# Performance work log

Hardware: AMD Instinct MI355X
Metric: run time of the kernel (lower is better)

## Reference

```python
import jax, jax.numpy as jnp
import numpy as np

NEG_INF = -9e15  # matches the torch -9000000000000000.0 mask value
LRELU_SLOPE = 0.01  # torch nn.LeakyReLU default


def setup_inputs() -> dict:
    key = jax.random.key(0)
    k1, k2, k3, k4 = jax.random.split(key, 4)
    N, F_in, F_out = 8192, 256, 128
    x = jax.random.normal(k1, (N, F_in), dtype=jnp.float32)
    adj = jax.random.randint(k2, (N, N), 0, 2, dtype=jnp.int32)
    # xavier_uniform with gain=1.414
    limW = 1.414 * np.sqrt(6.0 / (F_in + F_out))
    W = jax.random.uniform(k3, (F_in, F_out), minval=-limW, maxval=limW, dtype=jnp.float32)
    lima = 1.414 * np.sqrt(6.0 / (2 * F_out + 1))
    a = jax.random.uniform(k4, (2 * F_out, 1), minval=-lima, maxval=lima, dtype=jnp.float32)
    return {"x": x, "adj": adj, "W": W, "a": a}


def reference(x, adj, W, a):
    # h: [N, F_out]
    h = x @ W
    F_out = h.shape[1]
    a1 = a[:F_out, 0]   # attention vector for source node i
    a2 = a[F_out:, 0]   # attention vector for target node j
    # e[i, j] = leaky_relu(h_i . a1 + h_j . a2) -- equivalent to the repeat/cat
    # construction without materializing the [N, N, 2F] tensor.
    e = (h @ a1)[:, None] + (h @ a2)[None, :]  # [N, N]
    e = jnp.where(e > 0, e, LRELU_SLOPE * e)
    scores = jnp.where(adj > 0, e, NEG_INF)
    attention = jax.nn.softmax(scores, axis=1)  # dropout omitted (eval mode)
    h_prime = attention @ h  # [N, F_out]
    return jax.nn.elu(h_prime)
```

## Files before the change

kernel.cpp:

```cpp
#include <hip/hip_runtime.h>
#include <hip/hip_bf16.h>
#include <stdint.h>


#define N_NODES 8192
#define F_INF   256
#define F_OUT   128
#define LRELU   0.01f

typedef __bf16 bf16x8 __attribute__((ext_vector_type(8)));
typedef float  f32x4  __attribute__((ext_vector_type(4)));
using bf16 = __hip_bfloat16;

__device__ __forceinline__ float b2f(bf16 v) { return __bfloat162float(v); }
__device__ __forceinline__ bf16  f2b(float v) { return __float2bfloat16(v); }

__device__ __forceinline__ void gll16(const void* g, void* l) {
    __builtin_amdgcn_global_load_lds(
        (const __attribute__((address_space(1))) uint32_t*)g,
        (__attribute__((address_space(3))) uint32_t*)l, 16, 0, 0);
}

__global__ __launch_bounds__(256) void k_xw(const float* __restrict__ x,
                                            const float* __restrict__ W,
                                            const float* __restrict__ a,
                                            bf16* __restrict__ hT,
                                            float* __restrict__ s1,
                                            float* __restrict__ s2,
                                            float* __restrict__ mgp) {
    __shared__ __align__(16) bf16 WTh[F_OUT][F_INF + 8];
    __shared__ __align__(16) bf16 WTl[F_OUT][F_INF + 8];
    __shared__ __align__(16) bf16 XSh[32][72];
    __shared__ __align__(16) bf16 XSl[32][72];
    __shared__ float a1s[F_OUT], a2s[F_OUT], s1L[32], s2L[32];
    const int tid  = threadIdx.x;
    const int lane = tid & 63, wave = tid >> 6;
    const int i0   = blockIdx.x * 32;
    if (tid < F_OUT) { a1s[tid] = a[tid]; a2s[tid] = a[tid + F_OUT]; }
    if (tid < 32)    { s1L[tid] = 0.f; s2L[tid] = 0.f; }
    for (int idx = tid; idx < (F_INF * F_OUT) / 8; idx += 256) {
        int k  = idx >> 4;
        int n0 = (idx & 15) * 8;
        const float* src = W + (size_t)k * F_OUT + n0;
        float4 va = *(const float4*)(src);
        float4 vb = *(const float4*)(src + 4);
        float v[8] = {va.x, va.y, va.z, va.w, vb.x, vb.y, vb.z, vb.w};
#pragma unroll
        for (int c = 0; c < 8; ++c) {
            bf16 hi = f2b(v[c]);
            WTh[n0 + c][k] = hi;
            WTl[n0 + c][k] = f2b(v[c] - b2f(hi));
        }
    }
    __syncthreads();
    f32x4 acc[4];
#pragma unroll
    for (int t = 0; t < 4; ++t) acc[t] = {0.f, 0.f, 0.f, 0.f};
    const int m = lane & 15, quad = lane >> 4;
    const int rt = wave & 1, cH = wave >> 1;
    for (int kc = 0; kc < F_INF / 64; ++kc) {
        const int k0 = kc * 64;
        {
            int part = tid & 7;
            int r    = tid >> 3;
            const float* src = x + (size_t)(i0 + r) * F_INF + k0 + part * 8;
            float4 va = *(const float4*)(src);
            float4 vb = *(const float4*)(src + 4);
            float v[8] = {va.x, va.y, va.z, va.w, vb.x, vb.y, vb.z, vb.w};
            __align__(16) bf16 th[8];
            __align__(16) bf16 tl[8];
#pragma unroll
            for (int c = 0; c < 8; ++c) {
                bf16 hi = f2b(v[c]);
                th[c] = hi;
                tl[c] = f2b(v[c] - b2f(hi));
            }
            *(uint4*)(&XSh[r][part * 8]) = *(const uint4*)th;
            *(uint4*)(&XSl[r][part * 8]) = *(const uint4*)tl;
        }
        __syncthreads();
#pragma unroll
        for (int ks = 0; ks < 2; ++ks) {
            bf16x8 ah = *(const bf16x8*)(&XSh[rt * 16 + m][ks * 32 + quad * 8]);
            bf16x8 al = *(const bf16x8*)(&XSl[rt * 16 + m][ks * 32 + quad * 8]);
#pragma unroll
            for (int c = 0; c < 4; ++c) {
                const int ct = cH * 4 + c;
                bf16x8 bh = *(const bf16x8*)(&WTh[ct * 16 + m][k0 + ks * 32 + quad * 8]);
                bf16x8 bl = *(const bf16x8*)(&WTl[ct * 16 + m][k0 + ks * 32 + quad * 8]);
                acc[c] = __builtin_amdgcn_mfma_f32_16x16x32_bf16(al, bh, acc[c], 0, 0, 0);
                acc[c] = __builtin_amdgcn_mfma_f32_16x16x32_bf16(ah, bl, acc[c], 0, 0, 0);
                acc[c] = __builtin_amdgcn_mfma_f32_16x16x32_bf16(ah, bh, acc[c], 0, 0, 0);
            }
        }
        __syncthreads();
    }
    float p1[4] = {0.f, 0.f, 0.f, 0.f}, p2[4] = {0.f, 0.f, 0.f, 0.f};
#pragma unroll
    for (int c = 0; c < 4; ++c) {
        const int f = (cH * 4 + c) * 16 + m;
        const float w1 = a1s[f], w2 = a2s[f];
#pragma unroll
        for (int r = 0; r < 4; ++r) { p1[r] += acc[c][r] * w1; p2[r] += acc[c][r] * w2; }
    }
#pragma unroll
    for (int r = 0; r < 4; ++r) {
        const int row = rt * 16 + quad * 4 + r;
        atomicAdd(&s1L[row], p1[r]);
        atomicAdd(&s2L[row], p2[r]);
    }
#pragma unroll
    for (int c = 0; c < 4; ++c) {
        const int f = (cH * 4 + c) * 16 + m;
#pragma unroll
        for (int r = 0; r < 4; ++r) {
            const int i = i0 + rt * 16 + quad * 4 + r;
            hT[(size_t)f * N_NODES + i] = f2b(acc[c][r]);
        }
    }
    __syncthreads();
    if (tid < 32) {
        s1[i0 + tid] = s1L[tid];
        s2[i0 + tid] = s2L[tid];
        float m2 = s2L[tid];
#pragma unroll
        for (int s = 16; s > 0; s >>= 1) m2 = fmaxf(m2, __shfl_xor(m2, s));
        if (tid == 0) mgp[blockIdx.x] = m2;
    }
}

__global__ __launch_bounds__(256, 4) void k_attn(const int* __restrict__ adj,
                                                 const float* __restrict__ s1g,
                                                 const float* __restrict__ s2g,
                                                 const float* __restrict__ mgp,
                                                 const bf16* __restrict__ hT,
                                                 float* __restrict__ Of,
                                                 float* __restrict__ lp) {
    __shared__ __align__(16) bf16 HS2[2][F_OUT][64];
    __shared__ float wred[4];
    __shared__ float lsum[32];
    const int tid  = threadIdx.x;
    const int lane = tid & 63, wave = tid >> 6;
    const int m = lane & 15, quad = lane >> 4;
    const int rt = wave & 1, kh = wave >> 1;
    const int i0    = blockIdx.x * 32;
    const int jq    = blockIdx.y;
    const int jbase = jq * 2048;
    const int irow  = i0 + rt * 16 + m;
    const float s1v = s1g[irow];
    float mv = mgp[tid];
#pragma unroll
    for (int s = 32; s > 0; s >>= 1) mv = fmaxf(mv, __shfl_xor(mv, s));
    if (lane == 0) wred[wave] = mv;
    if (tid < 32) lsum[tid] = 0.f;
    const int part = tid & 7, fr = tid >> 3;
    const int psw  = (part ^ (fr & 7)) * 8;
    const bf16* hTp = hT + jbase + psw;
#pragma unroll
    for (int g = 0; g < 4; ++g)
        gll16(hTp + (size_t)(fr + g * 32) * N_NODES, &HS2[0][fr + g * 32][part * 8]);
    const int jloc = kh * 32 + quad * 8;
    const int4*   arowp = (const int4*)(adj + (size_t)irow * N_NODES + jbase);
    const float4* srowp = (const float4*)(s2g + jbase);
    int4   avA = arowp[jloc / 4],     avB = arowp[jloc / 4 + 1];
    float4 svA = srowp[jloc / 4],     svB = srowp[jloc / 4 + 1];
    float lacc = 0.f;
    f32x4 acc[8];
#pragma unroll
    for (int c = 0; c < 8; ++c) acc[c] = {0.f, 0.f, 0.f, 0.f};
    __syncthreads();
    const float mgv = fmaxf(fmaxf(wred[0], wred[1]), fmaxf(wred[2], wred[3]));
    const float tmi = s1v + mgv;
    const float mi  = fmaxf(tmi, LRELU * tmi);
    const int slotsw = ((kh * 4 + quad) ^ (m & 7)) * 8;

    for (int jc = 0; jc < 32; ++jc) {
        const int cur = jc & 1;
        if (jc < 31) {
#pragma unroll
            for (int g = 0; g < 4; ++g)
                gll16(hTp + (size_t)(fr + g * 32) * N_NODES + (jc + 1) * 64,
                      &HS2[cur ^ 1][fr + g * 32][part * 8]);
        }
        const int jn = (jc < 31) ? jc + 1 : 31;
        int4   navA = arowp[jn * 16 + jloc / 4], navB = arowp[jn * 16 + jloc / 4 + 1];
        float4 nsvA = srowp[jn * 16 + jloc / 4], nsvB = srowp[jn * 16 + jloc / 4 + 1];
        const int   am[8] = {avA.x, avA.y, avA.z, avA.w, avB.x, avB.y, avB.z, avB.w};
        const float sm[8] = {svA.x, svA.y, svA.z, svA.w, svB.x, svB.y, svB.z, svB.w};
        __align__(16) bf16 a8[8];
#pragma unroll
        for (int t = 0; t < 8; ++t) {
            float e = s1v + sm[t];
            e = fmaxf(e, LRELU * e);
            float w = (am[t] > 0) ? __expf(e - mi) : 0.f;
            bf16 b = f2b(w);
            a8[t] = b;
            lacc += b2f(b);
        }
        bf16x8 afrag = *(const bf16x8*)a8;
        __builtin_amdgcn_s_setprio(1);
#pragma unroll
        for (int c = 0; c < 8; ++c) {
            bf16x8 bfr = *(const bf16x8*)(&HS2[cur][c * 16 + m][slotsw]);
            acc[c] = __builtin_amdgcn_mfma_f32_16x16x32_bf16(afrag, bfr, acc[c], 0, 0, 0);
        }
        __builtin_amdgcn_s_setprio(0);
        avA = navA; avB = navB; svA = nsvA; svB = nsvB;
        __syncthreads();
    }
    lacc += __shfl_xor(lacc, 16);
    lacc += __shfl_xor(lacc, 32);
    if (quad == 0) atomicAdd(&lsum[rt * 16 + m], lacc);
    __syncthreads();
    if (tid < 32) lp[(size_t)jq * N_NODES + i0 + tid] = lsum[tid];
    float* scr = (float*)&HS2[0][0][0];
    if (kh == 1) {
#pragma unroll
        for (int c = 0; c < 8; ++c)
#pragma unroll
            for (int r = 0; r < 4; ++r)
                scr[(rt * 16 + quad * 4 + r) * 128 + c * 16 + m] = acc[c][r];
    }
    __syncthreads();
    if (kh == 0) {
#pragma unroll
        for (int c = 0; c < 8; ++c)
#pragma unroll
            for (int r = 0; r < 4; ++r) {
                const int row = rt * 16 + quad * 4 + r;
                const int f   = c * 16 + m;
                Of[((size_t)jq * N_NODES + i0 + row) * F_OUT + f] =
                    acc[c][r] + scr[row * 128 + f];
            }
    }
}

__global__ __launch_bounds__(256) void k_comb(const float* __restrict__ Of,
                                              const float* __restrict__ lp,
                                              float* __restrict__ out) {
    size_t gid = (size_t)blockIdx.x * 256 + threadIdx.x;
    int i = (int)(gid >> 7);
    float s = 0.f, l = 0.f;
#pragma unroll
    for (int q = 0; q < 4; ++q) {
        s += Of[(size_t)q * (N_NODES * (size_t)F_OUT) + gid];
        l += lp[q * N_NODES + i];
    }
    float o = s / l;
    out[gid] = o > 0.f ? o : __expf(o) - 1.f;
}

extern "C" void kernel_launch(void* const* d_in, const int* in_sizes, int n_in,
                              void* d_out, int out_size, void* d_ws, size_t ws_size,
                              hipStream_t stream) {
    (void)out_size; (void)ws_size;
    const float* x   = nullptr;
    const int*   adj = nullptr;
    const float* W   = nullptr;
    const float* a   = nullptr;
    for (int ii = 0; ii < n_in; ++ii) {
        int sz = in_sizes[ii];
        if      (sz == N_NODES * F_INF)  x   = (const float*)d_in[ii];
        else if (sz == F_INF * F_OUT)    W   = (const float*)d_in[ii];
        else if (sz == 2 * F_OUT)        a   = (const float*)d_in[ii];
        else                             adj = (const int*)d_in[ii];
    }
    float* out = (float*)d_out;

    char* ws = (char*)d_ws;
    bf16*  hT  = (bf16*)ws;  ws += (size_t)F_OUT * N_NODES * 2;
    float* s1  = (float*)ws; ws += N_NODES * 4;
    float* s2  = (float*)ws; ws += N_NODES * 4;
    float* mgp = (float*)ws; ws += 256 * 4;
    float* lp  = (float*)ws; ws += 4 * N_NODES * 4;
    float* Of  = (float*)ws;

    k_xw  <<<N_NODES / 32, 256, 0, stream>>>(x, W, a, hT, s1, s2, mgp);
    k_attn<<<dim3(N_NODES / 32, 4), 256, 0, stream>>>(adj, s1, s2, mgp, hT, Of, lp);
    k_comb<<<(N_NODES * F_OUT) / 256, 256, 0, stream>>>(Of, lp, out);
}
```

Measured before the change: 437.2 us.

## Pack adjacency into a bitmask in the projection kernel for attention

The projection kernel now also reads the int32 adjacency matrix and writes a 1-bit-per-edge mask, and the attention kernel reads that compact mask instead of int32 rows. The attention kernel's per-tile adjacency traffic shrinks and the register footprint of prefetched mask data drops. The full 256 MB adjacency read still happens once, now in the first kernel, and a 8 MB mask write plus read is added. The extra pass could lengthen the first kernel enough to cancel the gain.

```diff
diff --git a/kernel.cpp b/kernel.cpp
--- a/kernel.cpp
+++ b/kernel.cpp
@@ -24,10 +24,12 @@
 __global__ __launch_bounds__(256) void k_xw(const float* __restrict__ x,
                                             const float* __restrict__ W,
                                             const float* __restrict__ a,
+                                            const int* __restrict__ adjp,
                                             bf16* __restrict__ hT,
                                             float* __restrict__ s1,
                                             float* __restrict__ s2,
-                                            float* __restrict__ mgp) {
+                                            float* __restrict__ mgp,
+                                            uint32_t* __restrict__ mask) {
     __shared__ __align__(16) bf16 WTh[F_OUT][F_INF + 8];
     __shared__ __align__(16) bf16 WTl[F_OUT][F_INF + 8];
     __shared__ __align__(16) bf16 XSh[32][72];
@@ -127,9 +129,27 @@
         for (int s = 16; s > 0; s >>= 1) m2 = fmaxf(m2, __shfl_xor(m2, s));
         if (tid == 0) mgp[blockIdx.x] = m2;
     }
-}
-
-__global__ __launch_bounds__(256, 4) void k_attn(const int* __restrict__ adj,
+    {
+        const size_t base = (size_t)blockIdx.x * 8192 + tid;
+#pragma unroll 2
+        for (int k2 = 0; k2 < 32; ++k2) {
+            const size_t w = base + (size_t)k2 * 256;
+            const int4* p = (const int4*)(adjp + w * 32);
+            uint32_t b = 0;
+#pragma unroll
+            for (int g = 0; g < 8; ++g) {
+                int4 v = p[g];
+                b |= (uint32_t)(v.x > 0) << (g * 4 + 0);
+                b |= (uint32_t)(v.y > 0) << (g * 4 + 1);
+                b |= (uint32_t)(v.z > 0) << (g * 4 + 2);
+                b |= (uint32_t)(v.w > 0) << (g * 4 + 3);
+            }
+            mask[w] = b;
+        }
+    }
+}
+
+__global__ __launch_bounds__(256, 4) void k_attn(const uint32_t* __restrict__ mask,
                                                  const float* __restrict__ s1g,
                                                  const float* __restrict__ s2g,
                                                  const float* __restrict__ mgp,
@@ -160,10 +180,10 @@
     for (int g = 0; g < 4; ++g)
         gll16(hTp + (size_t)(fr + g * 32) * N_NODES, &HS2[0][fr + g * 32][part * 8]);
     const int jloc = kh * 32 + quad * 8;
-    const int4*   arowp = (const int4*)(adj + (size_t)irow * N_NODES + jbase);
-    const float4* srowp = (const float4*)(s2g + jbase);
-    int4   avA = arowp[jloc / 4],     avB = arowp[jloc / 4 + 1];
-    float4 svA = srowp[jloc / 4],     svB = srowp[jloc / 4 + 1];
+    const uint32_t* mrow = mask + (size_t)irow * (N_NODES / 32) + jq * 64;
+    const float4*  srowp = (const float4*)(s2g + jbase);
+    uint32_t mw = mrow[kh];
+    float4 svA = srowp[jloc / 4], svB = srowp[jloc / 4 + 1];
     float lacc = 0.f;
     f32x4 acc[8];
 #pragma unroll
@@ -183,16 +203,16 @@
                       &HS2[cur ^ 1][fr + g * 32][part * 8]);
         }
         const int jn = (jc < 31) ? jc + 1 : 31;
-        int4   navA = arowp[jn * 16 + jloc / 4], navB = arowp[jn * 16 + jloc / 4 + 1];
+        uint32_t nmw = mrow[jn * 2 + kh];
         float4 nsvA = srowp[jn * 16 + jloc / 4], nsvB = srowp[jn * 16 + jloc / 4 + 1];
-        const int   am[8] = {avA.x, avA.y, avA.z, avA.w, avB.x, avB.y, avB.z, avB.w};
         const float sm[8] = {svA.x, svA.y, svA.z, svA.w, svB.x, svB.y, svB.z, svB.w};
+        const uint32_t mb = (mw >> (quad * 8)) & 0xffu;
         __align__(16) bf16 a8[8];
 #pragma unroll
         for (int t = 0; t < 8; ++t) {
             float e = s1v + sm[t];
             e = fmaxf(e, LRELU * e);
-            float w = (am[t] > 0) ? __expf(e - mi) : 0.f;
+            float w = ((mb >> t) & 1u) ? __expf(e - mi) : 0.f;
             bf16 b = f2b(w);
             a8[t] = b;
             lacc += b2f(b);
@@ -205,7 +225,7 @@
             acc[c] = __builtin_amdgcn_mfma_f32_16x16x32_bf16(afrag, bfr, acc[c], 0, 0, 0);
         }
         __builtin_amdgcn_s_setprio(0);
-        avA = navA; avB = navB; svA = nsvA; svB = nsvB;
+        mw = nmw; svA = nsvA; svB = nsvB;
         __syncthreads();
     }
     lacc += __shfl_xor(lacc, 16);
@@ -268,14 +288,16 @@
     float* out = (float*)d_out;
 
     char* ws = (char*)d_ws;
-    bf16*  hT  = (bf16*)ws;  ws += (size_t)F_OUT * N_NODES * 2;
-    float* s1  = (float*)ws; ws += N_NODES * 4;
-    float* s2  = (float*)ws; ws += N_NODES * 4;
-    float* mgp = (float*)ws; ws += 256 * 4;
-    float* lp  = (float*)ws; ws += 4 * N_NODES * 4;
-    float* Of  = (float*)ws;
-
-    k_xw  <<<N_NODES / 32, 256, 0, stream>>>(x, W, a, hT, s1, s2, mgp);
-    k_attn<<<dim3(N_NODES / 32, 4), 256, 0, stream>>>(adj, s1, s2, mgp, hT, Of, lp);
+    bf16*     hT   = (bf16*)ws;     ws += (size_t)F_OUT * N_NODES * 2;
+    float*    s1   = (float*)ws;    ws += N_NODES * 4;
+    float*    s2   = (float*)ws;    ws += N_NODES * 4;
+    float*    mgp  = (float*)ws;    ws += 256 * 4;
+    float*    lp   = (float*)ws;    ws += 4 * N_NODES * 4;
+    uint32_t* mask = (uint32_t*)ws;
+    ws += (size_t)N_NODES * (N_NODES / 32) * sizeof(uint32_t);
+    float*    Of   = (float*)ws;
+
+    k_xw  <<<N_NODES / 32, 256, 0, stream>>>(x, W, a, adj, hT, s1, s2, mgp, mask);
+    k_attn<<<dim3(N_NODES / 32, 4), 256, 0, stream>>>(mask, s1, s2, mgp, hT, Of, lp);
     k_comb<<<(N_NODES * F_OUT) / 256, 256, 0, stream>>>(Of, lp, out);
 }
```

Measured after the change: 441.6 us. About the same (+1.0%).
